# Kernel tuning notes

Measured on AMD Instinct MI355X. Metric: run time of the kernel, lower is better.

Reference implementation:

```python
import jax, jax.numpy as jnp
import numpy as np

WS = 16; HEADS = 6; TOPK = 64; KIN = 128; EPS = 1e-10
B, C, H, W = 1, 192, 192, 192
HID = 4 * C  # mlp_ratio * dim


def _ln(x, g, b):
    m = jnp.mean(x, axis=-1, keepdims=True)
    v = jnp.var(x, axis=-1, keepdims=True)
    return (x - m) * jax.lax.rsqrt(v + 1e-5) * g + b


def _dw_gelu(x, hw, w, b):
    # depthwise 5x5 conv + exact GELU on token sequence (B, N, C)
    Bx, N, Cx = x.shape
    h, wd = hw
    xi = x.transpose(0, 2, 1).reshape(Bx, Cx, h, wd)
    y = jax.lax.conv_general_dilated(xi, w, (1, 1), 'SAME',
        feature_group_count=Cx, dimension_numbers=('NCHW', 'OIHW', 'NCHW'))
    y = jax.nn.gelu(y + b[None, :, None, None], approximate=False)
    return y.reshape(Bx, Cx, N).transpose(0, 2, 1)


def _window_partition(x):
    b, h, w, c = x.shape
    x = x.reshape(b, h // WS, WS, w // WS, WS, c)
    return x.transpose(0, 1, 3, 2, 4, 5).reshape(-1, WS * WS, c)


def _window_reverse(win, h, w):
    c = win.shape[-1]
    b = win.shape[0] // ((h // WS) * (w // WS))
    x = win.reshape(b, h // WS, w // WS, WS, WS, c)
    return x.transpose(0, 1, 3, 2, 4, 5).reshape(b, h, w, c)


def setup_inputs():
    key = jax.random.key(0)
    ks = jax.random.split(key, 16)
    b_, n = B * (H // WS) * (W // WS), WS * WS
    wgen = lambda k, sh: jax.random.normal(k, sh, jnp.float32) * 0.02
    p = {}
    p['features_mv'] = jax.random.normal(ks[0], (B, C, H, W), jnp.float32)
    p['pfa_values'] = jax.random.uniform(ks[1], (b_, HEADS, n, KIN), jnp.float32)
    p['pfa_indices'] = jax.random.randint(ks[2], (b_, HEADS, n, KIN), 0, n, jnp.int32)
    p['rpi'] = jax.random.randint(ks[3], (n, n), 0, (2 * WS - 1) ** 2, jnp.int32)
    p['ln1_g'] = jnp.ones((C,)); p['ln1_b'] = jnp.zeros((C,))
    p['Wq_w'] = wgen(ks[4], (C, C)); p['Wq_b'] = jnp.zeros((C,))
    p['Wk_w'] = wgen(ks[5], (C, C)); p['Wk_b'] = jnp.zeros((C,))
    p['Wv_w'] = wgen(ks[6], (C, C)); p['Wv_b'] = jnp.zeros((C,))
    p['lepe_w'] = wgen(ks[7], (C, 1, 5, 5)); p['lepe_b'] = jnp.zeros((C,))
    p['rpb_table'] = wgen(ks[8], ((2 * WS - 1) ** 2, HEADS))
    p['proj_w'] = wgen(ks[9], (C, C)); p['proj_b'] = jnp.zeros((C,))
    p['ln2_g'] = jnp.ones((C,)); p['ln2_b'] = jnp.zeros((C,))
    p['fc1_w'] = wgen(ks[10], (C, HID)); p['fc1_b'] = jnp.zeros((HID,))
    p['ffn_dw_w'] = wgen(ks[11], (HID, 1, 5, 5)); p['ffn_dw_b'] = jnp.zeros((HID,))
    p['fc2_w'] = wgen(ks[12], (HID, C)); p['fc2_b'] = jnp.zeros((C,))
    return p


def reference(features_mv, pfa_values, pfa_indices, rpi, ln1_g, ln1_b,
              Wq_w, Wq_b, Wk_w, Wk_b, Wv_w, Wv_b, lepe_w, lepe_b, rpb_table,
              proj_w, proj_b, ln2_g, ln2_b, fc1_w, fc1_b, ffn_dw_w, ffn_dw_b,
              fc2_w, fc2_b):
    b, c, h, w = features_mv.shape
    hd = c // HEADS
    x = features_mv.reshape(b, c, h * w).transpose(0, 2, 1)  # (B, HW, C)
    shortcut = x
    xn = _ln(x, ln1_g, ln1_b)
    q = xn @ Wq_w + Wq_b
    k = xn @ Wk_w + Wk_b
    v = xn @ Wv_w + Wv_b
    vl = _dw_gelu(v, (h, w), lepe_w, lepe_b)  # v_LePE
    qkvp = jnp.concatenate([q, k, v, vl], axis=-1).reshape(b, h, w, 4 * c)
    xw = _window_partition(qkvp)  # (b_, n, 4C)
    b_, n = xw.shape[0], WS * WS
    qkvp = xw.reshape(b_, n, 4, HEADS, hd).transpose(2, 0, 3, 1, 4)
    q, k, v, vl = qkvp[0] * hd ** -0.5, qkvp[1], qkvp[2], qkvp[3]
    # SMM_QmK: per-query gathered q.k — dense scores then index gather
    scores = jnp.einsum('bhid,bhjd->bhij', q, k)          # (b_, H, n, n)
    attn = jnp.take_along_axis(scores, pfa_indices, axis=-1)  # (b_, H, n, K)
    # relative position bias, gathered by the same sparse indices
    rpb = rpb_table[rpi.reshape(-1)].reshape(n, n, HEADS).transpose(2, 0, 1)
    rpb_g = jnp.take_along_axis(jnp.broadcast_to(rpb[None], (b_, HEADS, n, n)),
                                pfa_indices, axis=-1)
    attn = jax.nn.softmax(attn + rpb_g, axis=-1)
    # progressive focused attention: multiply by prior values, renormalize
    attn = attn * pfa_values
    attn = (attn + EPS) / (jnp.sum(attn, axis=-1, keepdims=True) + EPS)
    # in-layer top-k reselection (topk=64 < KIN=128)
    tv, ti = jax.lax.top_k(attn, TOPK)
    idx = jnp.take_along_axis(pfa_indices, ti, axis=-1)   # (b_, H, n, TOPK)
    # SMM_AmV: scatter sparse attn to dense (duplicates sum) then matmul
    BH = b_ * HEADS
    a = tv.reshape(BH, n, TOPK)
    idxf = idx.reshape(BH, n, TOPK)
    dense = jnp.zeros((BH, n, n), tv.dtype).at[
        jnp.arange(BH)[:, None, None], jnp.arange(n)[None, :, None], idxf].add(a)
    xo = jnp.einsum('bij,bjd->bid', dense, v.reshape(BH, n, hd))
    xo = xo.reshape(b_, HEADS, n, hd) + vl
    xo = xo.transpose(0, 2, 1, 3).reshape(b_, n, c) @ proj_w + proj_b
    xr = _window_reverse(xo.reshape(-1, WS, WS, c), h, w)
    x = shortcut + xr.reshape(b, h * w, c)
    # ConvFFN
    y = _ln(x, ln2_g, ln2_b) @ fc1_w + fc1_b
    y = jax.nn.gelu(y, approximate=False)
    y = y + _dw_gelu(y, (h, w), ffn_dw_w, ffn_dw_b)
    x = x + (y @ fc2_w + fc2_b)
    return x
```

## Files before the change

### kernel.cpp

```cpp
#include <hip/hip_runtime.h>
#include <math.h>

#define HW 36864
#define CD 192
#define NH 6
#define HDIM 32
#define HIDD 768

typedef unsigned short u16;
typedef __attribute__((ext_vector_type(8))) short bf16x8;
typedef __attribute__((ext_vector_type(4))) float f32x4;

__device__ __forceinline__ float gelu_f(float x) {
  return 0.5f * x * (1.0f + erff(x * 0.70710678118654752f));
}
__device__ __forceinline__ u16 f2b(float f) {
  union { float f; unsigned u; } v; v.f = f;
  unsigned r = v.u + 0x7fff + ((v.u >> 16) & 1);
  return (u16)(r >> 16);
}
__device__ __forceinline__ float b2f(u16 b) {
  union { unsigned u; float f; } v; v.u = ((unsigned)b) << 16;
  return v.f;
}
__device__ __forceinline__ float b2f_lo(unsigned u) {
  union { unsigned x; float f; } v; v.x = u << 16; return v.f;
}
__device__ __forceinline__ float b2f_hi(unsigned u) {
  union { unsigned x; float f; } v; v.x = u & 0xffff0000u; return v.f;
}

__global__ __launch_bounds__(256)
void lnt_kernel(const float* __restrict__ in, const float* __restrict__ g,
                const float* __restrict__ b, u16* __restrict__ outTM)
{
  __shared__ float tile[64][193];
  __shared__ float red[64][8];
  __shared__ float2 stat2[64];
  __shared__ float gb[384];
  const int tid = threadIdx.x;
  const int part = tid >> 6, tk = tid & 63;
  const int tok = blockIdx.x * 64 + tk;
  if (tid < 192) { gb[tid] = g[tid]; gb[192 + tid] = b[tid]; }
  float s = 0.f, sq = 0.f;
  for (int c = part * 48; c < part * 48 + 48; ++c) {
    float v = in[(size_t)c * HW + tok];
    tile[tk][c] = v; s += v; sq += v * v;
  }
  red[tk][part] = s; red[tk][4 + part] = sq;
  __syncthreads();
  if (tid < 64) {
    float ss = red[tid][0] + red[tid][1] + red[tid][2] + red[tid][3];
    float qq = red[tid][4] + red[tid][5] + red[tid][6] + red[tid][7];
    float m = ss * (1.0f / CD);
    float var = fmaxf(qq * (1.0f / CD) - m * m, 0.f);
    stat2[tid] = make_float2(m, rsqrtf(var + 1e-5f));
  }
  __syncthreads();
  unsigned* op = (unsigned*)outTM + (size_t)blockIdx.x * 6144;
  #pragma unroll
  for (int r = 0; r < 24; ++r) {
    int idx = tid + r * 256;
    int tok2 = idx / 96, dc = idx - tok2 * 96;
    float2 st = stat2[tok2];
    int c = dc * 2;
    float v0 = (tile[tok2][c] - st.x) * st.y * gb[c] + gb[192 + c];
    float v1 = (tile[tok2][c + 1] - st.x) * st.y * gb[c + 1] + gb[192 + c + 1];
    op[idx] = (unsigned)f2b(v0) | ((unsigned)f2b(v1) << 16);
  }
}

__global__ __launch_bounds__(256)
void wtrans_kernel(const float* __restrict__ in, u16* __restrict__ out, int K, int N)
{
  __shared__ float ls[32][33];
  const int k0 = blockIdx.x * 32, n0 = blockIdx.y * 32;
  const int t = threadIdx.x;
  #pragma unroll
  for (int r = 0; r < 4; ++r) {
    int idx = t + r * 256;
    int k = idx >> 5, n = idx & 31;
    ls[k][n] = in[(size_t)(k0 + k) * N + n0 + n];
  }
  __syncthreads();
  #pragma unroll
  for (int r = 0; r < 4; ++r) {
    int idx = t + r * 256;
    int n = idx >> 5, k = idx & 31;
    out[(size_t)(n0 + n) * K + k0 + k] = f2b(ls[k][n]);
  }
}

__global__ __launch_bounds__(256)
void wtrans4_kernel(const float* __restrict__ w0, const float* __restrict__ w1,
                    const float* __restrict__ w2, const float* __restrict__ w3,
                    u16* __restrict__ out)
{
  __shared__ float ls[32][33];
  const int z = blockIdx.z;
  const float* in = (z == 0) ? w0 : (z == 1 ? w1 : (z == 2 ? w2 : w3));
  u16* op = out + (size_t)z * CD * CD;
  const int k0 = blockIdx.x * 32, n0 = blockIdx.y * 32;
  const int t = threadIdx.x;
  #pragma unroll
  for (int r = 0; r < 4; ++r) {
    int idx = t + r * 256;
    int k = idx >> 5, n = idx & 31;
    ls[k][n] = in[(size_t)(k0 + k) * CD + n0 + n];
  }
  __syncthreads();
  #pragma unroll
  for (int r = 0; r < 4; ++r) {
    int idx = t + r * 256;
    int n = idx >> 5, k = idx & 31;
    op[(size_t)(n0 + n) * CD + k0 + k] = f2b(ls[k][n]);
  }
}

__global__ __launch_bounds__(256)
void rpbg_kernel(const int* __restrict__ rpi, const float* __restrict__ rpb_t,
                 float* __restrict__ out)
{
  const int i = blockIdx.x, j = threadIdx.x;
  const int r = rpi[i * 256 + j];
  #pragma unroll
  for (int h = 0; h < NH; ++h)
    out[(size_t)h * 65536 + i * 256 + j] = rpb_t[r * NH + h];
}

template<int MODE>
__global__ __launch_bounds__(256, 4)
void mgemm_kernel(const u16* __restrict__ A,
                  const u16* __restrict__ W0, const u16* __restrict__ W1, const u16* __restrict__ W2,
                  const float* __restrict__ b0, const float* __restrict__ b1, const float* __restrict__ b2,
                  const float* __restrict__ aux, void* __restrict__ outv,
                  int K, int segN)
{
  const int n0 = blockIdx.x * 64;
  const int m0 = blockIdx.y * 128;
  const int seg = n0 / segN;
  const u16* Wp = (seg == 0) ? W0 : (seg == 1 ? W1 : W2);
  const float* biasp = (seg == 0) ? b0 : (seg == 1 ? b1 : b2);
  const int nl0 = n0 - seg * segN;

  __shared__ u16 As[128 * 40];
  __shared__ u16 Bs[64 * 40];

  const int tid = threadIdx.x;
  const int lane = tid & 63, wave = tid >> 6;
  const int wm = (wave >> 1) * 64, wn = (wave & 1) * 32;
  const int fm = lane & 15, fq = lane >> 4;
  const int ar = tid >> 2, akq = tid & 3;

  f32x4 acc[4][2];
  #pragma unroll
  for (int i = 0; i < 4; ++i) { acc[i][0] = (f32x4)(0.f); acc[i][1] = (f32x4)(0.f); }

  uint4 rA0, rA1, rB, nA0, nA1, nB;
  rA0 = *(const uint4*)(A + (size_t)(m0 + ar) * K + akq * 8);
  rA1 = *(const uint4*)(A + (size_t)(m0 + ar + 64) * K + akq * 8);
  rB  = *(const uint4*)(Wp + (size_t)(nl0 + ar) * K + akq * 8);

  for (int k0 = 0; k0 < K; k0 += 32) {
    *(uint4*)(&As[ar * 40 + akq * 8]) = rA0;
    *(uint4*)(&As[(ar + 64) * 40 + akq * 8]) = rA1;
    *(uint4*)(&Bs[ar * 40 + akq * 8]) = rB;
    __syncthreads();
    const int kn = (k0 + 32 < K) ? k0 + 32 : k0;
    nA0 = *(const uint4*)(A + (size_t)(m0 + ar) * K + kn + akq * 8);
    nA1 = *(const uint4*)(A + (size_t)(m0 + ar + 64) * K + kn + akq * 8);
    nB  = *(const uint4*)(Wp + (size_t)(nl0 + ar) * K + kn + akq * 8);
    bf16x8 af[4], bf[2];
    #pragma unroll
    for (int mt = 0; mt < 4; ++mt)
      af[mt] = *(const bf16x8*)(&As[(wm + mt * 16 + fm) * 40 + fq * 8]);
    #pragma unroll
    for (int nt = 0; nt < 2; ++nt)
      bf[nt] = *(const bf16x8*)(&Bs[(wn + nt * 16 + fm) * 40 + fq * 8]);
    #pragma unroll
    for (int mt = 0; mt < 4; ++mt)
      #pragma unroll
      for (int nt = 0; nt < 2; ++nt)
        acc[mt][nt] = __builtin_amdgcn_mfma_f32_16x16x32_bf16(af[mt], bf[nt], acc[mt][nt], 0, 0, 0);
    __syncthreads();
    rA0 = nA0; rA1 = nA1; rB = nB;
  }

  #pragma unroll
  for (int nt = 0; nt < 2; ++nt) {
    const int n = n0 + wn + nt * 16 + fm;
    const float bia = biasp[nl0 + wn + nt * 16 + fm];
    #pragma unroll
    for (int mt = 0; mt < 4; ++mt) {
      const int mb = m0 + wm + mt * 16 + fq * 4;
      float o[4];
      #pragma unroll
      for (int r = 0; r < 4; ++r) o[r] = acc[mt][nt][r] + bia;
      if (MODE == 0) {
        const float sc = (seg == 0) ? 0.17677669529663689f : 1.0f;
        u16 h0 = f2b(o[0] * sc), h1 = f2b(o[1] * sc), h2 = f2b(o[2] * sc), h3 = f2b(o[3] * sc);
        uint2 pk = make_uint2((unsigned)h0 | ((unsigned)h1 << 16), (unsigned)h2 | ((unsigned)h3 << 16));
        *(uint2*)((u16*)outv + (size_t)n * HW + mb) = pk;
      } else if (MODE == 1) {
        const float4 ax = *(const float4*)(aux + (size_t)n * HW + mb);
        *(float4*)((float*)outv + (size_t)n * HW + mb) =
            make_float4(o[0] + ax.x, o[1] + ax.y, o[2] + ax.z, o[3] + ax.w);
      } else if (MODE == 2) {
        u16 h0 = f2b(gelu_f(o[0])), h1 = f2b(gelu_f(o[1]));
        u16 h2 = f2b(gelu_f(o[2])), h3 = f2b(gelu_f(o[3]));
        uint2 pk = make_uint2((unsigned)h0 | ((unsigned)h1 << 16), (unsigned)h2 | ((unsigned)h3 << 16));
        *(uint2*)((u16*)outv + (size_t)n * HW + mb) = pk;
      } else {
        const float4 ax = *(const float4*)(aux + (size_t)n * HW + mb);
        float* op = (float*)outv;
        op[(size_t)(mb + 0) * CD + n] = o[0] + ax.x;
        op[(size_t)(mb + 1) * CD + n] = o[1] + ax.y;
        op[(size_t)(mb + 2) * CD + n] = o[2] + ax.z;
        op[(size_t)(mb + 3) * CD + n] = o[3] + ax.w;
      }
    }
  }
}

template<bool ADD>
__global__ __launch_bounds__(256)
void dwconv_tm_kernel(const u16* __restrict__ in, const float* __restrict__ w,
                      const float* __restrict__ bias, u16* __restrict__ out, int PL)
{
  const int p0 = blockIdx.z * 32;
  const int bx = blockIdx.x * 64, by = blockIdx.y * 4;
  __shared__ u16 tile[32 * 546];
  __shared__ float ws[32][26];
  const int tid = threadIdx.x;
  for (int e = tid; e < 832; e += 256) {
    int p = e / 26, q = e - p * 26;
    ws[p][q] = (q < 25) ? w[(p0 + p) * 25 + q] : bias[p0 + p];
  }
  for (int e = tid; e < 256 * 34; e += 256) {
    int rp = e / 34, ch = e - rp * 34;
    int p = rp >> 3, r = rp & 7;
    int gy = by + r - 2, gx = bx + ch * 2 - 2;
    unsigned val = 0;
    if (gy >= 0 && gy < 192 && gx >= 0 && gx < 192)
      val = *(const unsigned*)(in + (size_t)(p0 + p) * HW + gy * 192 + gx);
    *(unsigned*)&tile[p * 546 + r * 68 + ch * 2] = val;
  }
  __syncthreads();
  const int txp = tid >> 3, pg = tid & 7;
  u16 res[4][2][4];
  #pragma unroll
  for (int pp = 0; pp < 4; ++pp) {
    const int p = pg * 4 + pp;
    const u16* tp = &tile[p * 546];
    float o0[4] = {0.f, 0.f, 0.f, 0.f}, o1[4] = {0.f, 0.f, 0.f, 0.f};
    #pragma unroll
    for (int ir = 0; ir < 8; ++ir) {
      const unsigned* rowp = (const unsigned*)(tp + ir * 68 + txp * 2);
      unsigned ua = rowp[0], ub = rowp[1], uc = rowp[2];
      float f0 = b2f_lo(ua), f1 = b2f_hi(ua), f2 = b2f_lo(ub);
      float f3 = b2f_hi(ub), f4 = b2f_lo(uc), f5 = b2f_hi(uc);
      #pragma unroll
      for (int dy = 0; dy < 5; ++dy) {
        const int r = ir - dy;
        if (r >= 0 && r < 4) {
          const float w0 = ws[p][dy * 5 + 0], w1 = ws[p][dy * 5 + 1], w2 = ws[p][dy * 5 + 2];
          const float w3 = ws[p][dy * 5 + 3], w4 = ws[p][dy * 5 + 4];
          o0[r] += f0 * w0 + f1 * w1 + f2 * w2 + f3 * w3 + f4 * w4;
          o1[r] += f1 * w0 + f2 * w1 + f3 * w2 + f4 * w3 + f5 * w4;
        }
      }
    }
    const float bb = ws[p][25];
    #pragma unroll
    for (int r = 0; r < 4; ++r) {
      float v0 = gelu_f(o0[r] + bb);
      float v1 = gelu_f(o1[r] + bb);
      if (ADD) {
        unsigned ctr = *(const unsigned*)(tp + (r + 2) * 68 + txp * 2 + 2);
        v0 += b2f_lo(ctr); v1 += b2f_hi(ctr);
      }
      res[pp][0][r] = f2b(v0); res[pp][1][r] = f2b(v1);
    }
  }
  #pragma unroll
  for (int r = 0; r < 4; ++r) {
    #pragma unroll
    for (int c = 0; c < 2; ++c) {
      const int pix = (by + r) * 192 + bx + txp * 2 + c;
      uint2 pk = make_uint2(
        (unsigned)res[0][c][r] | ((unsigned)res[1][c][r] << 16),
        (unsigned)res[2][c][r] | ((unsigned)res[3][c][r] << 16));
      *(uint2*)(out + (size_t)pix * PL + p0 + pg * 4) = pk;
    }
  }
}

__global__ __launch_bounds__(512, 4)
void attn_kernel(const u16* __restrict__ qg, const u16* __restrict__ kg,
                 const u16* __restrict__ vg, const u16* __restrict__ vlt,
                 const float* __restrict__ pfa_v, const int* __restrict__ pfa_i,
                 const float* __restrict__ rpbg, u16* __restrict__ attn_out)
{
  const int h = blockIdx.x;
  const int win = blockIdx.y;
  const int wy = (win / 12) * 16;
  const int wx = (win - (win / 12) * 12) * 16;
  const size_t hb = (size_t)h * HDIM * HW;

  __shared__ u16 kT[256 * 40];
  __shared__ u16 vJ[256 * 40];
  __shared__ float Sb[32 * 260];
  __shared__ u16 qT[32 * 40];
  __shared__ float2 selbuf[8][64];

  const int tid = threadIdx.x;
  const int lane = tid & 63, wave = tid >> 6;

  #pragma unroll
  for (int r = 0; r < 8; ++r) {
    int idx = tid + r * 512;
    int d = idx >> 7, jp = idx & 127, j = jp * 2;
    int pg = (wy + (j >> 4)) * 192 + (wx + (j & 15));
    ushort2 kv = *(const ushort2*)(kg + hb + (size_t)d * HW + pg);
    kT[j * 40 + d] = kv.x; kT[(j + 1) * 40 + d] = kv.y;
    ushort2 vv = *(const ushort2*)(vg + hb + (size_t)d * HW + pg);
    vJ[j * 40 + d] = vv.x; vJ[(j + 1) * 40 + d] = vv.y;
  }
  __syncthreads();

  const size_t wb = ((size_t)win * NH + h) * 256;
  const float* rpp = rpbg + (size_t)h * 65536;

  for (int pass = 0; pass < 8; ++pass) {
    {
      int d = tid >> 4, ip = tid & 15, i = pass * 32 + ip * 2;
      int pg = (wy + (i >> 4)) * 192 + (wx + (i & 15));
      ushort2 qv = *(const ushort2*)(qg + hb + (size_t)d * HW + pg);
      qT[(ip * 2) * 40 + d] = qv.x; qT[(ip * 2 + 1) * 40 + d] = qv.y;
    }
    __syncthreads();
    {
      const int it = wave & 1;
      const int fm = lane & 15, fq = lane >> 4;
      bf16x8 aq = *(const bf16x8*)&qT[(it * 16 + fm) * 40 + fq * 8];
      #pragma unroll
      for (int t = 0; t < 4; ++t) {
        int j0 = ((wave >> 1) * 4 + t) * 16;
        bf16x8 bk = *(const bf16x8*)&kT[(j0 + fm) * 40 + fq * 8];
        f32x4 c = __builtin_amdgcn_mfma_f32_16x16x32_bf16(aq, bk, (f32x4)(0.f), 0, 0, 0);
        const int col = j0 + fm, rowb = it * 16 + fq * 4;
        const int ib = pass * 32 + rowb;
        c[0] += rpp[(size_t)(ib + 0) * 256 + col];
        c[1] += rpp[(size_t)(ib + 1) * 256 + col];
        c[2] += rpp[(size_t)(ib + 2) * 256 + col];
        c[3] += rpp[(size_t)(ib + 3) * 256 + col];
        Sb[(rowb + 0) * 260 + col] = c[0]; Sb[(rowb + 1) * 260 + col] = c[1];
        Sb[(rowb + 2) * 260 + col] = c[2]; Sb[(rowb + 3) * 260 + col] = c[3];
      }
    }
    __syncthreads();
    int pj1[4], pj2[4]; float pv1[4], pv2[4];
    #pragma unroll
    for (int u = 0; u < 4; ++u) {
      const int i = pass * 32 + u * 8 + wave;
      const size_t base = (wb + (size_t)i) * 128;
      pj1[u] = pfa_i[base + lane];  pj2[u] = pfa_i[base + 64 + lane];
      pv1[u] = pfa_v[base + lane];  pv2[u] = pfa_v[base + 64 + lane];
    }
    #pragma unroll
    for (int u = 0; u < 4; ++u) {
      const int iq = u * 8 + wave;
      const int i  = pass * 32 + iq;
      const int j1 = pj1[u], j2 = pj2[u];
      float s1 = Sb[iq * 260 + j1];
      float s2 = Sb[iq * 260 + j2];
      float mx = fmaxf(s1, s2);
      #pragma unroll
      for (int o = 32; o > 0; o >>= 1) mx = fmaxf(mx, __shfl_xor(mx, o));
      float e1 = expf(s1 - mx), e2 = expf(s2 - mx);
      float u1 = e1 * pv1[u], u2 = e2 * pv2[u];
      const unsigned ub1 = __float_as_uint(u1), ub2 = __float_as_uint(u2);
      unsigned thr = 0u;
      for (int bit = 30; bit >= 0; --bit) {
        unsigned cand = thr | (1u << bit);
        int cnt = (int)__popcll(__ballot(ub1 >= cand)) + (int)__popcll(__ballot(ub2 >= cand));
        if (cnt >= 64) { thr = cand; if (cnt == 64) break; }
      }
      float sA = e1 + e2, sB = u1 + u2;
      #pragma unroll
      for (int o = 32; o > 0; o >>= 1) { sA += __shfl_xor(sA, o); sB += __shfl_xor(sB, o); }
      const unsigned long long lmlt = (1ull << lane) - 1ull;
      const bool gt1 = ub1 > thr, gt2 = ub2 > thr;
      const bool eq1 = ub1 == thr, eq2 = ub2 == thr;
      const unsigned long long meq1 = __ballot(eq1), meq2 = __ballot(eq2);
      const int need = 64 - (int)__popcll(__ballot(gt1)) - (int)__popcll(__ballot(gt2));
      const bool sel1 = gt1 || (eq1 && (int)__popcll(meq1 & lmlt) < need);
      const bool sel2 = gt2 || (eq2 && ((int)__popcll(meq1) + (int)__popcll(meq2 & lmlt)) < need);
      const unsigned long long ms1 = __ballot(sel1), ms2 = __ballot(sel2);
      const int pos1 = (int)__popcll(ms1 & lmlt);
      const int pos2 = (int)__popcll(ms1) + (int)__popcll(ms2 & lmlt);
      const float t = 1e-10f * sA;
      const float rden = 1.0f / (sB + t);
      if (sel1) selbuf[wave][pos1] = make_float2((u1 + t) * rden, __int_as_float(j1));
      if (sel2) selbuf[wave][pos2] = make_float2((u2 + t) * rden, __int_as_float(j2));
      const int d = lane & 31, half = lane >> 5;
      float acc = 0.f;
      #pragma unroll
      for (int c = 0; c < 4; ++c) {
        float2 sv[8];
        #pragma unroll
        for (int q4 = 0; q4 < 4; ++q4)
          *(float4*)&sv[q4 * 2] = *(const float4*)&selbuf[wave][half * 32 + c * 8 + q4 * 2];
        #pragma unroll
        for (int s = 0; s < 8; ++s)
          acc = fmaf(sv[s].x, b2f(vJ[__float_as_int(sv[s].y) * 40 + d]), acc);
      }
      acc += __shfl_xor(acc, 32);
      const int pg = (wy + (i >> 4)) * 192 + (wx + (i & 15));
      if (lane < 32) {
        float o = acc + b2f(vlt[(size_t)pg * CD + h * HDIM + d]);
        attn_out[(size_t)pg * CD + h * HDIM + d] = f2b(o);
      }
    }
    __syncthreads();
  }
}

extern "C" void kernel_launch(void* const* d_in, const int* in_sizes, int n_in,
                              void* d_out, int out_size, void* d_ws, size_t ws_size,
                              hipStream_t stream)
{
  (void)in_sizes; (void)n_in; (void)out_size; (void)ws_size;
  const float* features = (const float*)d_in[0];
  const float* pfa_v    = (const float*)d_in[1];
  const int*   pfa_i    = (const int*)d_in[2];
  const int*   rpi      = (const int*)d_in[3];
  const float* ln1_g    = (const float*)d_in[4];
  const float* ln1_b    = (const float*)d_in[5];
  const float* Wq_w     = (const float*)d_in[6];
  const float* Wq_b     = (const float*)d_in[7];
  const float* Wk_w     = (const float*)d_in[8];
  const float* Wk_b     = (const float*)d_in[9];
  const float* Wv_w     = (const float*)d_in[10];
  const float* Wv_b     = (const float*)d_in[11];
  const float* lepe_w   = (const float*)d_in[12];
  const float* lepe_b   = (const float*)d_in[13];
  const float* rpb_t    = (const float*)d_in[14];
  const float* proj_w   = (const float*)d_in[15];
  const float* proj_b   = (const float*)d_in[16];
  const float* ln2_g    = (const float*)d_in[17];
  const float* ln2_b    = (const float*)d_in[18];
  const float* fc1_w    = (const float*)d_in[19];
  const float* fc1_b    = (const float*)d_in[20];
  const float* dw_w     = (const float*)d_in[21];
  const float* dw_b     = (const float*)d_in[22];
  const float* fc2_w    = (const float*)d_in[23];
  const float* fc2_b    = (const float*)d_in[24];

  char* ws = (char*)d_ws;
  const size_t S  = (size_t)HW * CD;
  const size_t SB = S * 4;
  u16*   xnt    = (u16*)(ws);
  u16*   qkvb   = (u16*)(ws + SB / 2);
  u16*   q_ = qkvb; u16* k_ = qkvb + S; u16* v_ = qkvb + 2 * S;
  u16*   vlt    = (u16*)(ws + 2 * SB);
  u16*   attn_o = (u16*)(ws + 2 * SB + SB / 2);
  float* x2     = (float*)(ws + 3 * SB);
  u16*   xn2t   = (u16*)(ws + 4 * SB);
  u16*   y_     = (u16*)(ws + 4 * SB + SB / 2);
  u16*   y2t    = (u16*)(ws + 6 * SB + SB / 2);
  u16*   wqt  = (u16*)(ws + 8 * SB + SB / 2);
  u16*   wkt  = wqt + 36864;
  u16*   wvt  = wkt + 36864;
  u16*   wpt  = wvt + 36864;
  u16*   wf1t = wpt + 36864;
  u16*   wf2t = wf1t + 147456;
  float* rpbg = (float*)(wf2t + 147456 + 128);
  float* out = (float*)d_out;

  wtrans4_kernel<<<dim3(6, 6, 4), 256, 0, stream>>>(Wq_w, Wk_w, Wv_w, proj_w, wqt);
  wtrans_kernel<<<dim3(6, 24), 256, 0, stream>>>(fc1_w, wf1t, 192, 768);
  wtrans_kernel<<<dim3(24, 6), 256, 0, stream>>>(fc2_w, wf2t, 768, 192);
  rpbg_kernel<<<dim3(256), 256, 0, stream>>>(rpi, rpb_t, rpbg);
  lnt_kernel<<<dim3(HW / 64), 256, 0, stream>>>(features, ln1_g, ln1_b, xnt);
  mgemm_kernel<0><<<dim3(9, HW / 128), 256, 0, stream>>>(xnt, wqt, wkt, wvt, Wq_b, Wk_b, Wv_b,
                                                         nullptr, qkvb, 192, 192);
  dwconv_tm_kernel<false><<<dim3(3, 48, 6), 256, 0, stream>>>(v_, lepe_w, lepe_b, vlt, CD);
  attn_kernel<<<dim3(6, 144), 512, 0, stream>>>(q_, k_, v_, vlt, pfa_v, pfa_i, rpbg, attn_o);
  mgemm_kernel<1><<<dim3(3, HW / 128), 256, 0, stream>>>(attn_o, wpt, wpt, wpt, proj_b, proj_b, proj_b,
                                                         features, x2, 192, 1 << 30);
  lnt_kernel<<<dim3(HW / 64), 256, 0, stream>>>(x2, ln2_g, ln2_b, xn2t);
  mgemm_kernel<2><<<dim3(12, HW / 128), 256, 0, stream>>>(xn2t, wf1t, wf1t, wf1t, fc1_b, fc1_b, fc1_b,
                                                          nullptr, y_, 192, 1 << 30);
  dwconv_tm_kernel<true><<<dim3(3, 48, 24), 256, 0, stream>>>(y_, dw_w, dw_b, y2t, HIDD);
  mgemm_kernel<3><<<dim3(3, HW / 128), 256, 0, stream>>>(y2t, wf2t, wf2t, wf2t, fc2_b, fc2_b, fc2_b,
                                                         x2, out, 768, 1 << 30);
}
```

Baseline: 800.7 us.

## Batch top-k selection across rows, prefetch PFA data, stage FFN output via LDS

```diff
diff --git a/kernel.cpp b/kernel.cpp
--- a/kernel.cpp
+++ b/kernel.cpp
@@ -128,13 +128,12 @@
     out[(size_t)h * 65536 + i * 256 + j] = rpb_t[r * NH + h];
 }
 
-template<int MODE>
+template<int MODE, int KK>
 __global__ __launch_bounds__(256, 4)
 void mgemm_kernel(const u16* __restrict__ A,
                   const u16* __restrict__ W0, const u16* __restrict__ W1, const u16* __restrict__ W2,
                   const float* __restrict__ b0, const float* __restrict__ b1, const float* __restrict__ b2,
-                  const float* __restrict__ aux, void* __restrict__ outv,
-                  int K, int segN)
+                  const float* __restrict__ aux, void* __restrict__ outv, int segN)
 {
   const int n0 = blockIdx.x * 64;
   const int m0 = blockIdx.y * 128;
@@ -157,19 +156,20 @@
   for (int i = 0; i < 4; ++i) { acc[i][0] = (f32x4)(0.f); acc[i][1] = (f32x4)(0.f); }
 
   uint4 rA0, rA1, rB, nA0, nA1, nB;
-  rA0 = *(const uint4*)(A + (size_t)(m0 + ar) * K + akq * 8);
-  rA1 = *(const uint4*)(A + (size_t)(m0 + ar + 64) * K + akq * 8);
-  rB  = *(const uint4*)(Wp + (size_t)(nl0 + ar) * K + akq * 8);
-
-  for (int k0 = 0; k0 < K; k0 += 32) {
+  rA0 = *(const uint4*)(A + (size_t)(m0 + ar) * KK + akq * 8);
+  rA1 = *(const uint4*)(A + (size_t)(m0 + ar + 64) * KK + akq * 8);
+  rB  = *(const uint4*)(Wp + (size_t)(nl0 + ar) * KK + akq * 8);
+
+  #pragma unroll
+  for (int k0 = 0; k0 < KK; k0 += 32) {
     *(uint4*)(&As[ar * 40 + akq * 8]) = rA0;
     *(uint4*)(&As[(ar + 64) * 40 + akq * 8]) = rA1;
     *(uint4*)(&Bs[ar * 40 + akq * 8]) = rB;
     __syncthreads();
-    const int kn = (k0 + 32 < K) ? k0 + 32 : k0;
-    nA0 = *(const uint4*)(A + (size_t)(m0 + ar) * K + kn + akq * 8);
-    nA1 = *(const uint4*)(A + (size_t)(m0 + ar + 64) * K + kn + akq * 8);
-    nB  = *(const uint4*)(Wp + (size_t)(nl0 + ar) * K + kn + akq * 8);
+    const int kn = (k0 + 32 < KK) ? k0 + 32 : k0;
+    nA0 = *(const uint4*)(A + (size_t)(m0 + ar) * KK + kn + akq * 8);
+    nA1 = *(const uint4*)(A + (size_t)(m0 + ar + 64) * KK + kn + akq * 8);
+    nB  = *(const uint4*)(Wp + (size_t)(nl0 + ar) * KK + kn + akq * 8);
     bf16x8 af[4], bf[2];
     #pragma unroll
     for (int mt = 0; mt < 4; ++mt)
@@ -186,37 +186,59 @@
     rA0 = nA0; rA1 = nA1; rB = nB;
   }
 
-  #pragma unroll
-  for (int nt = 0; nt < 2; ++nt) {
-    const int n = n0 + wn + nt * 16 + fm;
-    const float bia = biasp[nl0 + wn + nt * 16 + fm];
-    #pragma unroll
-    for (int mt = 0; mt < 4; ++mt) {
-      const int mb = m0 + wm + mt * 16 + fq * 4;
-      float o[4];
-      #pragma unroll
-      for (int r = 0; r < 4; ++r) o[r] = acc[mt][nt][r] + bia;
-      if (MODE == 0) {
-        const float sc = (seg == 0) ? 0.17677669529663689f : 1.0f;
-        u16 h0 = f2b(o[0] * sc), h1 = f2b(o[1] * sc), h2 = f2b(o[2] * sc), h3 = f2b(o[3] * sc);
-        uint2 pk = make_uint2((unsigned)h0 | ((unsigned)h1 << 16), (unsigned)h2 | ((unsigned)h3 << 16));
-        *(uint2*)((u16*)outv + (size_t)n * HW + mb) = pk;
-      } else if (MODE == 1) {
+  if constexpr (MODE == 3) {
+    __shared__ float Ts[128][65];
+    #pragma unroll
+    for (int nt = 0; nt < 2; ++nt) {
+      const int n = n0 + wn + nt * 16 + fm;
+      const float bia = biasp[nl0 + wn + nt * 16 + fm];
+      const int nl = wn + nt * 16 + fm;
+      #pragma unroll
+      for (int mt = 0; mt < 4; ++mt) {
+        const int mb = m0 + wm + mt * 16 + fq * 4;
+        const int ml = wm + mt * 16 + fq * 4;
         const float4 ax = *(const float4*)(aux + (size_t)n * HW + mb);
-        *(float4*)((float*)outv + (size_t)n * HW + mb) =
-            make_float4(o[0] + ax.x, o[1] + ax.y, o[2] + ax.z, o[3] + ax.w);
-      } else if (MODE == 2) {
-        u16 h0 = f2b(gelu_f(o[0])), h1 = f2b(gelu_f(o[1]));
-        u16 h2 = f2b(gelu_f(o[2])), h3 = f2b(gelu_f(o[3]));
-        uint2 pk = make_uint2((unsigned)h0 | ((unsigned)h1 << 16), (unsigned)h2 | ((unsigned)h3 << 16));
-        *(uint2*)((u16*)outv + (size_t)n * HW + mb) = pk;
-      } else {
-        const float4 ax = *(const float4*)(aux + (size_t)n * HW + mb);
-        float* op = (float*)outv;
-        op[(size_t)(mb + 0) * CD + n] = o[0] + ax.x;
-        op[(size_t)(mb + 1) * CD + n] = o[1] + ax.y;
-        op[(size_t)(mb + 2) * CD + n] = o[2] + ax.z;
-        op[(size_t)(mb + 3) * CD + n] = o[3] + ax.w;
+        Ts[ml + 0][nl] = acc[mt][nt][0] + bia + ax.x;
+        Ts[ml + 1][nl] = acc[mt][nt][1] + bia + ax.y;
+        Ts[ml + 2][nl] = acc[mt][nt][2] + bia + ax.z;
+        Ts[ml + 3][nl] = acc[mt][nt][3] + bia + ax.w;
+      }
+    }
+    __syncthreads();
+    float* op = (float*)outv;
+    #pragma unroll
+    for (int r = 0; r < 8; ++r) {
+      const int m = (tid >> 4) + r * 16;
+      const int c = (tid & 15) * 4;
+      float4 vv = make_float4(Ts[m][c], Ts[m][c + 1], Ts[m][c + 2], Ts[m][c + 3]);
+      *(float4*)(op + (size_t)(m0 + m) * CD + n0 + c) = vv;
+    }
+  } else {
+    #pragma unroll
+    for (int nt = 0; nt < 2; ++nt) {
+      const int n = n0 + wn + nt * 16 + fm;
+      const float bia = biasp[nl0 + wn + nt * 16 + fm];
+      #pragma unroll
+      for (int mt = 0; mt < 4; ++mt) {
+        const int mb = m0 + wm + mt * 16 + fq * 4;
+        float o[4];
+        #pragma unroll
+        for (int r = 0; r < 4; ++r) o[r] = acc[mt][nt][r] + bia;
+        if (MODE == 0) {
+          const float sc = (seg == 0) ? 0.17677669529663689f : 1.0f;
+          u16 h0 = f2b(o[0] * sc), h1 = f2b(o[1] * sc), h2 = f2b(o[2] * sc), h3 = f2b(o[3] * sc);
+          uint2 pk = make_uint2((unsigned)h0 | ((unsigned)h1 << 16), (unsigned)h2 | ((unsigned)h3 << 16));
+          *(uint2*)((u16*)outv + (size_t)n * HW + mb) = pk;
+        } else if (MODE == 1) {
+          const float4 ax = *(const float4*)(aux + (size_t)n * HW + mb);
+          *(float4*)((float*)outv + (size_t)n * HW + mb) =
+              make_float4(o[0] + ax.x, o[1] + ax.y, o[2] + ax.z, o[3] + ax.w);
+        } else {
+          u16 h0 = f2b(gelu_f(o[0])), h1 = f2b(gelu_f(o[1]));
+          u16 h2 = f2b(gelu_f(o[2])), h3 = f2b(gelu_f(o[3]));
+          uint2 pk = make_uint2((unsigned)h0 | ((unsigned)h1 << 16), (unsigned)h2 | ((unsigned)h3 << 16));
+          *(uint2*)((u16*)outv + (size_t)n * HW + mb) = pk;
+        }
       }
     }
   }
@@ -337,6 +359,14 @@
       int pg = (wy + (i >> 4)) * 192 + (wx + (i & 15));
       ushort2 qv = *(const ushort2*)(qg + hb + (size_t)d * HW + pg);
       qT[(ip * 2) * 40 + d] = qv.x; qT[(ip * 2 + 1) * 40 + d] = qv.y;
+    }
+    int pj1[4], pj2[4]; float pv1[4], pv2[4];
+    #pragma unroll
+    for (int u = 0; u < 4; ++u) {
+      const int i = pass * 32 + u * 8 + wave;
+      const size_t base = (wb + (size_t)i) * 128;
+      pj1[u] = pfa_i[base + lane];  pj2[u] = pfa_i[base + 64 + lane];
+      pv1[u] = pfa_v[base + lane];  pv2[u] = pfa_v[base + 64 + lane];
     }
     __syncthreads();
     {
@@ -359,39 +389,53 @@
       }
     }
     __syncthreads();
-    int pj1[4], pj2[4]; float pv1[4], pv2[4];
+
+    float s1[4], s2[4];
+    #pragma unroll
+    for (int u = 0; u < 4; ++u) {
+      const int iq = u * 8 + wave;
+      s1[u] = Sb[iq * 260 + pj1[u]];
+      s2[u] = Sb[iq * 260 + pj2[u]];
+    }
+    float mx[4];
+    #pragma unroll
+    for (int u = 0; u < 4; ++u) mx[u] = fmaxf(s1[u], s2[u]);
+    #pragma unroll
+    for (int o = 32; o > 0; o >>= 1) {
+      #pragma unroll
+      for (int u = 0; u < 4; ++u) mx[u] = fmaxf(mx[u], __shfl_xor(mx[u], o));
+    }
+    float e1[4], e2[4], u1[4], u2[4], sA[4], sB[4];
+    unsigned ub1[4], ub2[4];
+    #pragma unroll
+    for (int u = 0; u < 4; ++u) {
+      e1[u] = expf(s1[u] - mx[u]); e2[u] = expf(s2[u] - mx[u]);
+      u1[u] = e1[u] * pv1[u];      u2[u] = e2[u] * pv2[u];
+      sA[u] = e1[u] + e2[u];       sB[u] = u1[u] + u2[u];
+      ub1[u] = __float_as_uint(u1[u]); ub2[u] = __float_as_uint(u2[u]);
+    }
+    #pragma unroll
+    for (int o = 32; o > 0; o >>= 1) {
+      #pragma unroll
+      for (int u = 0; u < 4; ++u) { sA[u] += __shfl_xor(sA[u], o); sB[u] += __shfl_xor(sB[u], o); }
+    }
+    unsigned thr[4] = {0u, 0u, 0u, 0u};
+    for (int bit = 30; bit >= 0; --bit) {
+      #pragma unroll
+      for (int u = 0; u < 4; ++u) {
+        const unsigned cand = thr[u] | (1u << bit);
+        const int cnt = (int)__popcll(__ballot(ub1[u] >= cand)) +
+                        (int)__popcll(__ballot(ub2[u] >= cand));
+        thr[u] = (cnt >= 64) ? cand : thr[u];
+      }
+    }
+    const unsigned long long lmlt = (1ull << lane) - 1ull;
     #pragma unroll
     for (int u = 0; u < 4; ++u) {
       const int i = pass * 32 + u * 8 + wave;
-      const size_t base = (wb + (size_t)i) * 128;
-      pj1[u] = pfa_i[base + lane];  pj2[u] = pfa_i[base + 64 + lane];
-      pv1[u] = pfa_v[base + lane];  pv2[u] = pfa_v[base + 64 + lane];
-    }
-    #pragma unroll
-    for (int u = 0; u < 4; ++u) {
-      const int iq = u * 8 + wave;
-      const int i  = pass * 32 + iq;
       const int j1 = pj1[u], j2 = pj2[u];
-      float s1 = Sb[iq * 260 + j1];
-      float s2 = Sb[iq * 260 + j2];
-      float mx = fmaxf(s1, s2);
-      #pragma unroll
-      for (int o = 32; o > 0; o >>= 1) mx = fmaxf(mx, __shfl_xor(mx, o));
-      float e1 = expf(s1 - mx), e2 = expf(s2 - mx);
-      float u1 = e1 * pv1[u], u2 = e2 * pv2[u];
-      const unsigned ub1 = __float_as_uint(u1), ub2 = __float_as_uint(u2);
-      unsigned thr = 0u;
-      for (int bit = 30; bit >= 0; --bit) {
-        unsigned cand = thr | (1u << bit);
-        int cnt = (int)__popcll(__ballot(ub1 >= cand)) + (int)__popcll(__ballot(ub2 >= cand));
-        if (cnt >= 64) { thr = cand; if (cnt == 64) break; }
-      }
-      float sA = e1 + e2, sB = u1 + u2;
-      #pragma unroll
-      for (int o = 32; o > 0; o >>= 1) { sA += __shfl_xor(sA, o); sB += __shfl_xor(sB, o); }
-      const unsigned long long lmlt = (1ull << lane) - 1ull;
-      const bool gt1 = ub1 > thr, gt2 = ub2 > thr;
-      const bool eq1 = ub1 == thr, eq2 = ub2 == thr;
+      const bool gt1 = ub1[u] > thr[u], gt2 = ub2[u] > thr[u];
+      const bool eq1 = ub1[u] == thr[u], eq2 = ub2[u] == thr[u];
       const unsigned long long meq1 = __ballot(eq1), meq2 = __ballot(eq2);
       const int need = 64 - (int)__popcll(__ballot(gt1)) - (int)__popcll(__ballot(gt2));
       const bool sel1 = gt1 || (eq1 && (int)__popcll(meq1 & lmlt) < need);
@@ -399,10 +443,10 @@
       const unsigned long long ms1 = __ballot(sel1), ms2 = __ballot(sel2);
       const int pos1 = (int)__popcll(ms1 & lmlt);
       const int pos2 = (int)__popcll(ms1) + (int)__popcll(ms2 & lmlt);
-      const float t = 1e-10f * sA;
-      const float rden = 1.0f / (sB + t);
-      if (sel1) selbuf[wave][pos1] = make_float2((u1 + t) * rden, __int_as_float(j1));
-      if (sel2) selbuf[wave][pos2] = make_float2((u2 + t) * rden, __int_as_float(j2));
+      const float t = 1e-10f * sA[u];
+      const float rden = 1.0f / (sB[u] + t);
+      if (sel1) selbuf[wave][pos1] = make_float2((u1[u] + t) * rden, __int_as_float(j1));
+      if (sel2) selbuf[wave][pos2] = make_float2((u2[u] + t) * rden, __int_as_float(j2));
       const int d = lane & 31, half = lane >> 5;
       float acc = 0.f;
       #pragma unroll
@@ -483,16 +527,16 @@
   wtrans_kernel<<<dim3(24, 6), 256, 0, stream>>>(fc2_w, wf2t, 768, 192);
   rpbg_kernel<<<dim3(256), 256, 0, stream>>>(rpi, rpb_t, rpbg);
   lnt_kernel<<<dim3(HW / 64), 256, 0, stream>>>(features, ln1_g, ln1_b, xnt);
-  mgemm_kernel<0><<<dim3(9, HW / 128), 256, 0, stream>>>(xnt, wqt, wkt, wvt, Wq_b, Wk_b, Wv_b,
-                                                         nullptr, qkvb, 192, 192);
+  mgemm_kernel<0, 192><<<dim3(9, HW / 128), 256, 0, stream>>>(xnt, wqt, wkt, wvt, Wq_b, Wk_b, Wv_b,
+                                                              nullptr, qkvb, 192);
   dwconv_tm_kernel<false><<<dim3(3, 48, 6), 256, 0, stream>>>(v_, lepe_w, lepe_b, vlt, CD);
   attn_kernel<<<dim3(6, 144), 512, 0, stream>>>(q_, k_, v_, vlt, pfa_v, pfa_i, rpbg, attn_o);
-  mgemm_kernel<1><<<dim3(3, HW / 128), 256, 0, stream>>>(attn_o, wpt, wpt, wpt, proj_b, proj_b, proj_b,
-                                                         features, x2, 192, 1 << 30);
+  mgemm_kernel<1, 192><<<dim3(3, HW / 128), 256, 0, stream>>>(attn_o, wpt, wpt, wpt, proj_b, proj_b, proj_b,
+                                                              features, x2, 1 << 30);
   lnt_kernel<<<dim3(HW / 64), 256, 0, stream>>>(x2, ln2_g, ln2_b, xn2t);
-  mgemm_kernel<2><<<dim3(12, HW / 128), 256, 0, stream>>>(xn2t, wf1t, wf1t, wf1t, fc1_b, fc1_b, fc1_b,
-                                                          nullptr, y_, 192, 1 << 30);
+  mgemm_kernel<2, 192><<<dim3(12, HW / 128), 256, 0, stream>>>(xn2t, wf1t, wf1t, wf1t, fc1_b, fc1_b, fc1_b,
+                                                               nullptr, y_, 1 << 30);
   dwconv_tm_kernel<true><<<dim3(3, 48, 24), 256, 0, stream>>>(y_, dw_w, dw_b, y2t, HIDD);
-  mgemm_kernel<3><<<dim3(3, HW / 128), 256, 0, stream>>>(y2t, wf2t, wf2t, wf2t, fc2_b, fc2_b, fc2_b,
-                                                         x2, out, 768, 1 << 30);
-}
+  mgemm_kernel<3, 768><<<dim3(3, HW / 128), 256, 0, stream>>>(y2t, wf2t, wf2t, wf2t, fc2_b, fc2_b, fc2_b,
+                                                              x2, out, 1 << 30);
+}
```

Result: slower. 821.4 us (+2.6%).
